# Performance work log

Measured on AMD Instinct MI355X. Metric: run time of the kernel, lower is better.

The kernel has to match this reference:

```python
import jax, jax.numpy as jnp
import numpy as np

DIM = 1024
H = 16          # num query heads
KV = 8          # num kv heads
HD = DIM // H   # head_dim = 64
B, P = 8, 1024


def setup_inputs() -> dict:
    key = jax.random.key(0)
    ks = jax.random.split(key, 6)
    s = 0.02
    return {
        "x": jax.random.normal(ks[0], (B, P, DIM), dtype=jnp.float32),
        "Wq": jax.random.normal(ks[1], (DIM, DIM), dtype=jnp.float32) * s,
        "Wk": jax.random.normal(ks[2], (KV * HD, DIM), dtype=jnp.float32) * s,
        "Wv": jax.random.normal(ks[3], (KV * HD, DIM), dtype=jnp.float32) * s,
        "Wp": jax.random.normal(ks[4], (DIM, DIM), dtype=jnp.float32) * s,
        "bp": jax.random.normal(ks[5], (DIM,), dtype=jnp.float32) * s,
    }


def _q_allocations(k):
    # k: (B, KV, P, HD). k_norms: frobenius norm over (P, HD), summed over batch.
    kn = jnp.sqrt(jnp.sum(k * k, axis=(2, 3))).sum(axis=0)  # (KV,)
    kn = (kn - kn.min()) / (kn.max() - kn.min())
    alloc = jnp.round(kn / kn.sum() * H).astype(jnp.int32)   # (KV,)
    # fix up so alloc.sum() == H (mirrors the torch while-loops)
    alloc = jax.lax.while_loop(lambda a: a.sum() > H,
                               lambda a: a.at[jnp.argmax(a)].add(-1), alloc)
    alloc = jax.lax.while_loop(lambda a: a.sum() < H,
                               lambda a: a.at[jnp.argmin(a)].add(1), alloc)
    return alloc


def reference(x, Wq, Wk, Wv, Wp, bp):
    Bx, Px, C = x.shape
    scale = HD ** -0.5
    q = (x @ Wq.T).reshape(Bx, Px, H, HD).transpose(0, 2, 1, 3) * scale  # (B,H,P,HD)
    k = (x @ Wk.T).reshape(Bx, Px, KV, HD).transpose(0, 2, 1, 3)         # (B,KV,P,HD)
    v = (x @ Wv.T).reshape(Bx, Px, KV, HD).transpose(0, 2, 1, 3)

    alloc = _q_allocations(k)  # (KV,) sums to H
    # query head h belongs to kv group i where cumsum[i-1] <= h < cumsum[i].
    # Equivalent to torch.split(q, alloc) + per-group attention, because the
    # per-group softmax over keys is independent per query head.
    kv_idx = jnp.searchsorted(jnp.cumsum(alloc), jnp.arange(H), side='right')
    k_g = jnp.take(k, kv_idx, axis=1)  # (B,H,P,HD)
    v_g = jnp.take(v, kv_idx, axis=1)

    scores = jnp.einsum('bhqd,bhkd->bhqk', q, k_g)
    weights = jax.nn.softmax(scores, axis=-1)
    out = jnp.einsum('bhqk,bhkd->bhqd', weights, v_g)  # (B,H,P,HD)
    out = out.transpose(0, 2, 1, 3).reshape(Bx, Px, C)
    return out @ Wp.T + bp
```

## Files before the change

### kernel.cpp

```cpp
#include <hip/hip_runtime.h>
#include <stdint.h>


typedef float f32x4 __attribute__((ext_vector_type(4)));
typedef short s16x8 __attribute__((ext_vector_type(8)));
typedef short s16x4 __attribute__((ext_vector_type(4)));
typedef int   i32x4 __attribute__((ext_vector_type(4)));

__device__ __forceinline__ unsigned short f2bf(float f) {
  unsigned int u = __builtin_bit_cast(unsigned int, f);
  u = (u + 0x7FFFu + ((u >> 16) & 1u)) >> 16;
  return (unsigned short)u;
}

__device__ __forceinline__ unsigned int pk_bf16(float a, float b) {
#if __has_builtin(__builtin_amdgcn_cvt_pk_bf16_f32)
  auto v = __builtin_amdgcn_cvt_pk_bf16_f32(a, b);
  return __builtin_bit_cast(unsigned int, v);
#else
  unsigned int ua = __builtin_bit_cast(unsigned int, a);
  unsigned int ub = __builtin_bit_cast(unsigned int, b);
  ua += 0x7FFFu + ((ua >> 16) & 1u);
  ub += 0x7FFFu + ((ub >> 16) & 1u);
#if __has_builtin(__builtin_amdgcn_perm)
  return __builtin_amdgcn_perm(ub, ua, 0x07060302);
#else
  return (ua >> 16) | (ub & 0xFFFF0000u);
#endif
#endif
}

__device__ __forceinline__ unsigned int perm_half(unsigned int hi, unsigned int lo, int takeHi) {
#if __has_builtin(__builtin_amdgcn_perm)
  return __builtin_amdgcn_perm(hi, lo, takeHi ? 0x07060302u : 0x05040100u);
#else
  return takeHi ? ((lo >> 16) | (hi & 0xFFFF0000u)) : ((lo & 0xFFFFu) | (hi << 16));
#endif
}

__device__ __forceinline__ float fast_exp2(float x) {
#if __has_builtin(__builtin_amdgcn_exp2f)
  return __builtin_amdgcn_exp2f(x);
#else
  return exp2f(x);
#endif
}

#if __has_builtin(__builtin_amdgcn_global_load_lds)
#define HAVE_GLL 1
typedef const __attribute__((address_space(1))) void* gas_ptr;
typedef __attribute__((address_space(3))) void* las_ptr;
__device__ __forceinline__ void gll16(const void* g, void* l) {
  __builtin_amdgcn_global_load_lds((gas_ptr)g, (las_ptr)l, 16, 0, 0);
}
#endif

__global__ void convert_kernel(const float* __restrict__ x, const float* __restrict__ Wq,
                               const float* __restrict__ Wk, const float* __restrict__ Wv,
                               const float* __restrict__ Wp,
                               unsigned short* __restrict__ xb,
                               unsigned short* __restrict__ wqkv,
                               unsigned short* __restrict__ wpb,
                               float* __restrict__ sums) {
  if (blockIdx.x == 0 && threadIdx.x < 64) sums[threadIdx.x] = 0.0f;
  const long i = ((long)blockIdx.x * 256 + threadIdx.x) * 4;
  const float* src; unsigned short* dst; long off; float scale = 1.0f;
  if (i < 8388608L)       { src = x;  dst = xb;             off = i;             }
  else if (i < 9437184L)  { src = Wq; dst = wqkv;           off = i - 8388608L;  scale = 0.18033688011112042f; }
  else if (i < 9961472L)  { src = Wk; dst = wqkv + 1048576; off = i - 9437184L;  }
  else if (i < 10485760L) { src = Wv; dst = wqkv + 1572864; off = i - 9961472L;  }
  else                    { src = Wp; dst = wpb;            off = i - 10485760L; }
  f32x4 v = *(const f32x4*)(src + off);
  s16x4 o;
  o[0] = (short)f2bf(v[0] * scale);
  o[1] = (short)f2bf(v[1] * scale);
  o[2] = (short)f2bf(v[2] * scale);
  o[3] = (short)f2bf(v[3] * scale);
  *(s16x4*)(dst + off) = o;
}

template<int N, bool OUT_BF16, bool DO_SUMSQ>
__global__ __launch_bounds__(256)
void gemm_bt(const unsigned short* __restrict__ A,
             const unsigned short* __restrict__ Bw,
             unsigned short* __restrict__ Cb,
             float* __restrict__ Cf,
             const float* __restrict__ bias,
             float* __restrict__ sums) {
  __shared__ __align__(16) unsigned short As[8192];
  __shared__ __align__(16) unsigned short Bs[8192];
  constexpr int NB = N / 128;
  const int bm = blockIdx.x / NB, bn = blockIdx.x % NB;
  const int m0 = bm * 128, n0 = bn * 128;
  const int t = threadIdx.x;
  const int w = t >> 6, lane = t & 63, quad = lane >> 4, ln = lane & 15;
  const int wm = w & 1, wn = w >> 1;

  const int lrow = lane >> 3;
  const int lc8  = ((lane & 7) ^ lrow) << 3;
  const unsigned short* agl = A  + (m0 + w * 32 + lrow) * 1024 + lc8;
  const unsigned short* bgl = Bw + (n0 + w * 32 + lrow) * 1024 + lc8;

  f32x4 acc[4][4] = {};

  for (int k0 = 0; k0 < 1024; k0 += 64) {
    __syncthreads();
#ifdef HAVE_GLL
    #pragma unroll
    for (int c = 0; c < 4; ++c) {
      gll16(agl + k0 + c * 8192, &As[w * 2048 + c * 512]);
      gll16(bgl + k0 + c * 8192, &Bs[w * 2048 + c * 512]);
    }
#else
    i32x4 ra[4], rb[4];
    #pragma unroll
    for (int c = 0; c < 4; ++c) {
      ra[c] = *(const i32x4*)(agl + k0 + c * 8192);
      rb[c] = *(const i32x4*)(bgl + k0 + c * 8192);
    }
    #pragma unroll
    for (int c = 0; c < 4; ++c) {
      *(i32x4*)(&As[w * 2048 + c * 512 + lane * 8]) = ra[c];
      *(i32x4*)(&Bs[w * 2048 + c * 512 + lane * 8]) = rb[c];
    }
#endif
    __syncthreads();
    #pragma unroll
    for (int kc = 0; kc < 2; ++kc) {
      const int pcs = ((kc * 4 + quad) ^ (ln & 7)) << 3;
      s16x8 af[4], bf[4];
      #pragma unroll
      for (int i = 0; i < 4; ++i)
        af[i] = *(const s16x8*)(&As[(wm * 64 + i * 16 + ln) * 64 + pcs]);
      #pragma unroll
      for (int j = 0; j < 4; ++j)
        bf[j] = *(const s16x8*)(&Bs[(wn * 64 + j * 16 + ln) * 64 + pcs]);
      #pragma unroll
      for (int i = 0; i < 4; ++i)
        #pragma unroll
        for (int j = 0; j < 4; ++j)
          acc[i][j] = __builtin_amdgcn_mfma_f32_16x16x32_bf16(af[i], bf[j], acc[i][j], 0, 0, 0);
    }
  }

  if constexpr (DO_SUMSQ) {
    if (bn >= 8 && bn < 12) {
      float ss = 0.0f;
      #pragma unroll
      for (int i = 0; i < 4; ++i)
        #pragma unroll
        for (int j = 0; j < 4; ++j)
          #pragma unroll
          for (int r = 0; r < 4; ++r)
            ss += acc[i][j][r] * acc[i][j][r];
      #pragma unroll
      for (int off = 1; off < 64; off <<= 1) ss += __shfl_xor(ss, off);
      if (lane == 0)
        atomicAdd(&sums[(m0 >> 10) * 8 + (bn - 8) * 2 + wn], ss);
    }
  }

  #pragma unroll
  for (int j = 0; j < 4; ++j) {
    const int gn = n0 + wn * 64 + j * 16 + ln;
    float bv = 0.0f;
    if constexpr (!OUT_BF16) bv = bias[gn];
    #pragma unroll
    for (int i = 0; i < 4; ++i) {
      const int gm0 = m0 + wm * 64 + i * 16 + quad * 4;
      #pragma unroll
      for (int r = 0; r < 4; ++r) {
        float v = acc[i][j][r];
        if constexpr (OUT_BF16) Cb[(gm0 + r) * N + gn] = f2bf(v);
        else                    Cf[(gm0 + r) * N + gn] = v + bv;
      }
    }
  }
}

__global__ __launch_bounds__(256, 4)
void attn_kernel(const unsigned short* __restrict__ qkv,
                 const float* __restrict__ sums,
                 unsigned short* __restrict__ att) {
  __shared__ __align__(16) unsigned short Ks[4096];
  __shared__ __align__(16) unsigned short Vt[64][72];
  __shared__ __align__(16) unsigned int  Plb[4][32][36];
  __shared__ int kvs;

  const int bid = blockIdx.x;
  const int h = bid & 15, qt = (bid >> 4) & 7, b = bid >> 7;
  const int t = threadIdx.x, w = t >> 6, lane = t & 63, quad = lane >> 4, ln = lane & 15;

  if (t == 0) {
    float kn[8];
    for (int kv = 0; kv < 8; ++kv) {
      float s = 0.0f;
      for (int bb = 0; bb < 8; ++bb) s += sqrtf(sums[bb * 8 + kv]);
      kn[kv] = s;
    }
    float mn = kn[0], mx = kn[0];
    for (int i = 1; i < 8; ++i) { mn = fminf(mn, kn[i]); mx = fmaxf(mx, kn[i]); }
    float tot = 0.0f;
    for (int i = 0; i < 8; ++i) { kn[i] = (kn[i] - mn) / (mx - mn); tot += kn[i]; }
    int a[8], sum = 0;
    for (int i = 0; i < 8; ++i) { a[i] = (int)rintf(kn[i] * 16.0f / tot); sum += a[i]; }
    while (sum > 16) {
      int im = 0;
      for (int i = 1; i < 8; ++i) if (a[i] > a[im]) im = i;
      a[im]--; sum--;
    }
    while (sum < 16) {
      int im = 0;
      for (int i = 1; i < 8; ++i) if (a[i] < a[im]) im = i;
      a[im]++; sum++;
    }
    int cum = 0, idx = 0, c[8];
    for (int i = 0; i < 8; ++i) { cum += a[i]; c[i] = cum; }
    while (c[idx] <= h) idx++;
    kvs = idx;
  }
  __syncthreads();
  const int kvi = kvs;

  s16x8 qf[2][2];
  #pragma unroll
  for (int s = 0; s < 2; ++s) {
    const unsigned short* qp = qkv + (b * 1024 + qt * 128 + s * 64 + w * 16 + ln) * 2048
                               + h * 64 + quad * 8;
    qf[s][0] = *(const s16x8*)(qp);
    qf[s][1] = *(const s16x8*)(qp + 32);
  }

  const int lc8 = ((lane & 7) ^ (lane >> 3)) << 3;
  const unsigned short* kglA = qkv + (b * 1024 + w * 16 + (lane >> 3)) * 2048
                               + 1024 + kvi * 64 + lc8;
  const unsigned short* kglB = kglA + 8 * 2048;

  const int kp = t & 31, vd0 = (t >> 5) << 3;
  const unsigned short* vbase = qkv + (b * 1024 + 2 * kp) * 2048 + 1536 + kvi * 64 + vd0;

  s16x8 ones;
  #pragma unroll
  for (int j = 0; j < 8; ++j) ones[j] = (short)0x3F80;

  f32x4 Oa[2][4] = {};
  f32x4 lacc[2] = {};

  s16x8 va0 = *(const s16x8*)(vbase);
  s16x8 va1 = *(const s16x8*)(vbase + 2048);

  for (int kt = 0; kt < 16; ++kt) {
    __syncthreads();
#ifdef HAVE_GLL
    gll16(kglA + kt * 131072, Ks + w * 1024);
    gll16(kglB + kt * 131072, Ks + w * 1024 + 512);
#else
    i32x4 t0 = *(const i32x4*)(kglA + kt * 131072);
    i32x4 t1 = *(const i32x4*)(kglB + kt * 131072);
    *(i32x4*)(Ks + w * 1024 + lane * 8) = t0;
    *(i32x4*)(Ks + w * 1024 + 512 + lane * 8) = t1;
#endif
    #pragma unroll
    for (int i = 0; i < 8; ++i) {
      unsigned int pk = (unsigned int)(unsigned short)va0[i] |
                        ((unsigned int)(unsigned short)va1[i] << 16);
      *(unsigned int*)(&Vt[vd0 + i][2 * kp]) = pk;
    }
    __syncthreads();

    if (kt < 15) {
      const unsigned short* q = vbase + (kt + 1) * 131072;
      va0 = *(const s16x8*)(q);
      va1 = *(const s16x8*)(q + 2048);
    }

    s16x8 kfr[2][4];
    #pragma unroll
    for (int ks = 0; ks < 4; ++ks) {
      const int r0 = (ks * 16 + ln) * 64;
      kfr[0][ks] = *(const s16x8*)(Ks + r0 + (((quad    ) ^ (ln & 7)) << 3));
      kfr[1][ks] = *(const s16x8*)(Ks + r0 + (((quad + 4) ^ (ln & 7)) << 3));
    }

    #pragma unroll
    for (int s = 0; s < 2; ++s) {
      f32x4 sacc[4] = {};
      #pragma unroll
      for (int ks = 0; ks < 4; ++ks) {
        sacc[ks] = __builtin_amdgcn_mfma_f32_16x16x32_bf16(qf[s][0], kfr[0][ks], sacc[ks], 0, 0, 0);
        sacc[ks] = __builtin_amdgcn_mfma_f32_16x16x32_bf16(qf[s][1], kfr[1][ks], sacc[ks], 0, 0, 0);
      }
      #pragma unroll
      for (int r = 0; r < 4; ++r) {
        unsigned int d0 = pk_bf16(fast_exp2(sacc[0][r]), fast_exp2(sacc[1][r]));
        unsigned int d1 = pk_bf16(fast_exp2(sacc[2][r]), fast_exp2(sacc[3][r]));
        unsigned int* pr = &Plb[w][s * 16 + quad * 4 + r][0];
        pr[ln]      = d0;
        pr[ln + 16] = d1;
      }
    }
    __asm__ volatile("s_waitcnt lgkmcnt(0)" ::: "memory");

    #pragma unroll
    for (int kc = 0; kc < 2; ++kc) {
      s16x8 pf[2];
      #pragma unroll
      for (int s = 0; s < 2; ++s) {
        const unsigned int* base = &Plb[w][s * 16 + ln][kc * 16 + (quad & 1) * 8];
        i32x4 u0 = *(const i32x4*)(base);
        i32x4 u1 = *(const i32x4*)(base + 4);
        const int th = quad >> 1;
        i32x4 pp;
        pp[0] = (int)perm_half((unsigned)u0[1], (unsigned)u0[0], th);
        pp[1] = (int)perm_half((unsigned)u0[3], (unsigned)u0[2], th);
        pp[2] = (int)perm_half((unsigned)u1[1], (unsigned)u1[0], th);
        pp[3] = (int)perm_half((unsigned)u1[3], (unsigned)u1[2], th);
        pf[s] = __builtin_bit_cast(s16x8, pp);
      }
      #pragma unroll
      for (int ds = 0; ds < 4; ++ds) {
        s16x8 vf = *(const s16x8*)(&Vt[ds * 16 + ln][kc * 32 + quad * 8]);
        Oa[0][ds] = __builtin_amdgcn_mfma_f32_16x16x32_bf16(pf[0], vf, Oa[0][ds], 0, 0, 0);
        Oa[1][ds] = __builtin_amdgcn_mfma_f32_16x16x32_bf16(pf[1], vf, Oa[1][ds], 0, 0, 0);
      }
      lacc[0] = __builtin_amdgcn_mfma_f32_16x16x32_bf16(pf[0], ones, lacc[0], 0, 0, 0);
      lacc[1] = __builtin_amdgcn_mfma_f32_16x16x32_bf16(pf[1], ones, lacc[1], 0, 0, 0);
    }
  }

  #pragma unroll
  for (int s = 0; s < 2; ++s) {
    float inv[4];
    #pragma unroll
    for (int r = 0; r < 4; ++r) inv[r] = 1.0f / lacc[s][r];
    const int orow = b * 1024 + qt * 128 + s * 64 + w * 16 + quad * 4;
    #pragma unroll
    for (int ds = 0; ds < 4; ++ds)
      #pragma unroll
      for (int r = 0; r < 4; ++r)
        att[(orow + r) * 1024 + h * 64 + ds * 16 + ln] = f2bf(Oa[s][ds][r] * inv[r]);
  }
}

extern "C" void kernel_launch(void* const* d_in, const int* in_sizes, int n_in,
                              void* d_out, int out_size, void* d_ws, size_t ws_size,
                              hipStream_t stream) {
  const float* x  = (const float*)d_in[0];
  const float* Wq = (const float*)d_in[1];
  const float* Wk = (const float*)d_in[2];
  const float* Wv = (const float*)d_in[3];
  const float* Wp = (const float*)d_in[4];
  const float* bp = (const float*)d_in[5];

  char* ws = (char*)d_ws;
  unsigned short* xb   = (unsigned short*)(ws);
  unsigned short* wqkv = (unsigned short*)(ws + 16777216);
  unsigned short* wpb  = (unsigned short*)(ws + 20971520);
  unsigned short* qkv  = (unsigned short*)(ws + 23068672);
  float*          sums = (float*)(ws + 56623104);
  unsigned short* att  = xb;

  convert_kernel<<<11264, 256, 0, stream>>>(x, Wq, Wk, Wv, Wp, xb, wqkv, wpb, sums);
  gemm_bt<2048, true, true><<<1024, 256, 0, stream>>>(xb, wqkv, qkv, nullptr, nullptr, sums);
  attn_kernel<<<1024, 256, 0, stream>>>(qkv, sums, att);
  gemm_bt<1024, false, false><<<512, 256, 0, stream>>>(att, wpb, nullptr, (float*)d_out, bp, nullptr);
}
```

Baseline: 221.3 us.

## Double-buffer K and V tiles in attention kernel shared memory

Splits the K and transposed-V shared-memory tiles into two buffers so the next key tile's global loads and the V transpose writes are issued before computing on the current tile. The loop needs one barrier per iteration instead of two, and global-to-LDS traffic can overlap with the MFMA work. In exchange LDS use rises and the launch-bounds occupancy hint drops from 4 to 3 blocks per CU, which may lower latency hiding across waves.

```diff
diff --git a/kernel.cpp b/kernel.cpp
--- a/kernel.cpp
+++ b/kernel.cpp
@@ -178,12 +178,12 @@
   }
 }
 
-__global__ __launch_bounds__(256, 4)
+__global__ __launch_bounds__(256, 3)
 void attn_kernel(const unsigned short* __restrict__ qkv,
                  const float* __restrict__ sums,
                  unsigned short* __restrict__ att) {
-  __shared__ __align__(16) unsigned short Ks[4096];
-  __shared__ __align__(16) unsigned short Vt[64][72];
+  __shared__ __align__(16) unsigned short Ks[2][4096];
+  __shared__ __align__(16) unsigned short Vt[2][64][72];
   __shared__ __align__(16) unsigned int  Plb[4][32][36];
   __shared__ int kvs;
 
@@ -248,38 +248,59 @@
 
   s16x8 va0 = *(const s16x8*)(vbase);
   s16x8 va1 = *(const s16x8*)(vbase + 2048);
+#ifdef HAVE_GLL
+  gll16(kglA, &Ks[0][w * 1024]);
+  gll16(kglB, &Ks[0][w * 1024 + 512]);
+#else
+  {
+    i32x4 t0 = *(const i32x4*)(kglA);
+    i32x4 t1 = *(const i32x4*)(kglB);
+    *(i32x4*)(&Ks[0][w * 1024 + lane * 8]) = t0;
+    *(i32x4*)(&Ks[0][w * 1024 + 512 + lane * 8]) = t1;
+  }
+#endif
+  #pragma unroll
+  for (int i = 0; i < 8; ++i) {
+    unsigned int pk = (unsigned int)(unsigned short)va0[i] |
+                      ((unsigned int)(unsigned short)va1[i] << 16);
+    *(unsigned int*)(&Vt[0][vd0 + i][2 * kp]) = pk;
+  }
+  va0 = *(const s16x8*)(vbase + 131072);
+  va1 = *(const s16x8*)(vbase + 131072 + 2048);
+  __syncthreads();
 
   for (int kt = 0; kt < 16; ++kt) {
-    __syncthreads();
+    const int p = kt & 1, np = p ^ 1;
+
+    if (kt < 15) {
 #ifdef HAVE_GLL
-    gll16(kglA + kt * 131072, Ks + w * 1024);
-    gll16(kglB + kt * 131072, Ks + w * 1024 + 512);
-#else
-    i32x4 t0 = *(const i32x4*)(kglA + kt * 131072);
-    i32x4 t1 = *(const i32x4*)(kglB + kt * 131072);
-    *(i32x4*)(Ks + w * 1024 + lane * 8) = t0;
-    *(i32x4*)(Ks + w * 1024 + 512 + lane * 8) = t1;
-#endif
-    #pragma unroll
-    for (int i = 0; i < 8; ++i) {
-      unsigned int pk = (unsigned int)(unsigned short)va0[i] |
-                        ((unsigned int)(unsigned short)va1[i] << 16);
-      *(unsigned int*)(&Vt[vd0 + i][2 * kp]) = pk;
-    }
-    __syncthreads();
-
-    if (kt < 15) {
-      const unsigned short* q = vbase + (kt + 1) * 131072;
-      va0 = *(const s16x8*)(q);
-      va1 = *(const s16x8*)(q + 2048);
+      gll16(kglA + (kt + 1) * 131072, &Ks[np][w * 1024]);
+      gll16(kglB + (kt + 1) * 131072, &Ks[np][w * 1024 + 512]);
+#else
+      i32x4 t0 = *(const i32x4*)(kglA + (kt + 1) * 131072);
+      i32x4 t1 = *(const i32x4*)(kglB + (kt + 1) * 131072);
+      *(i32x4*)(&Ks[np][w * 1024 + lane * 8]) = t0;
+      *(i32x4*)(&Ks[np][w * 1024 + 512 + lane * 8]) = t1;
+#endif
+      #pragma unroll
+      for (int i = 0; i < 8; ++i) {
+        unsigned int pk = (unsigned int)(unsigned short)va0[i] |
+                          ((unsigned int)(unsigned short)va1[i] << 16);
+        *(unsigned int*)(&Vt[np][vd0 + i][2 * kp]) = pk;
+      }
+      if (kt < 14) {
+        const unsigned short* q = vbase + (kt + 2) * 131072;
+        va0 = *(const s16x8*)(q);
+        va1 = *(const s16x8*)(q + 2048);
+      }
     }
 
     s16x8 kfr[2][4];
     #pragma unroll
     for (int ks = 0; ks < 4; ++ks) {
       const int r0 = (ks * 16 + ln) * 64;
-      kfr[0][ks] = *(const s16x8*)(Ks + r0 + (((quad    ) ^ (ln & 7)) << 3));
-      kfr[1][ks] = *(const s16x8*)(Ks + r0 + (((quad + 4) ^ (ln & 7)) << 3));
+      kfr[0][ks] = *(const s16x8*)(&Ks[p][r0 + (((quad    ) ^ (ln & 7)) << 3)]);
+      kfr[1][ks] = *(const s16x8*)(&Ks[p][r0 + (((quad + 4) ^ (ln & 7)) << 3)]);
     }
 
     #pragma unroll
@@ -319,13 +340,15 @@
       }
       #pragma unroll
       for (int ds = 0; ds < 4; ++ds) {
-        s16x8 vf = *(const s16x8*)(&Vt[ds * 16 + ln][kc * 32 + quad * 8]);
+        s16x8 vf = *(const s16x8*)(&Vt[p][ds * 16 + ln][kc * 32 + quad * 8]);
         Oa[0][ds] = __builtin_amdgcn_mfma_f32_16x16x32_bf16(pf[0], vf, Oa[0][ds], 0, 0, 0);
         Oa[1][ds] = __builtin_amdgcn_mfma_f32_16x16x32_bf16(pf[1], vf, Oa[1][ds], 0, 0, 0);
       }
       lacc[0] = __builtin_amdgcn_mfma_f32_16x16x32_bf16(pf[0], ones, lacc[0], 0, 0, 0);
       lacc[1] = __builtin_amdgcn_mfma_f32_16x16x32_bf16(pf[1], ones, lacc[1], 0, 0, 0);
     }
+
+    __syncthreads();
   }
 
   #pragma unroll
```

New measurement: 226.3 us. 1.02x slower.

## Compute transposed attention scores so P feeds PV MFMA straight from registers

Applied to the files above, without the earlier changes.

Swaps the MFMA operand order so S^T and O^T come out in registers in a layout that can feed the PV product directly. The per-wave LDS round trip for the probability matrix (Plb buffer, waitcnt, perm shuffles) goes away. To make this work, K rows are permuted when loaded into LDS. The output store becomes packed 8-byte bf16 writes per lane. This removes LDS traffic and the extra sync inside each key tile, but the correctness of the row permutation mapping is a risk.

```diff
diff --git a/kernel.cpp b/kernel.cpp
--- a/kernel.cpp
+++ b/kernel.cpp
@@ -3,6 +3,7 @@
 
 
 typedef float f32x4 __attribute__((ext_vector_type(4)));
+typedef int   i32x2 __attribute__((ext_vector_type(2)));
 typedef short s16x8 __attribute__((ext_vector_type(8)));
 typedef short s16x4 __attribute__((ext_vector_type(4)));
 typedef int   i32x4 __attribute__((ext_vector_type(4)));
@@ -27,14 +28,6 @@
 #else
   return (ua >> 16) | (ub & 0xFFFF0000u);
 #endif
-#endif
-}
-
-__device__ __forceinline__ unsigned int perm_half(unsigned int hi, unsigned int lo, int takeHi) {
-#if __has_builtin(__builtin_amdgcn_perm)
-  return __builtin_amdgcn_perm(hi, lo, takeHi ? 0x07060302u : 0x05040100u);
-#else
-  return takeHi ? ((lo >> 16) | (hi & 0xFFFF0000u)) : ((lo & 0xFFFFu) | (hi << 16));
 #endif
 }
 
@@ -184,7 +177,6 @@
                  unsigned short* __restrict__ att) {
   __shared__ __align__(16) unsigned short Ks[4096];
   __shared__ __align__(16) unsigned short Vt[64][72];
-  __shared__ __align__(16) unsigned int  Plb[4][32][36];
   __shared__ int kvs;
 
   const int bid = blockIdx.x;
@@ -232,9 +224,12 @@
   }
 
   const int lc8 = ((lane & 7) ^ (lane >> 3)) << 3;
-  const unsigned short* kglA = qkv + (b * 1024 + w * 16 + (lane >> 3)) * 2048
-                               + 1024 + kvi * 64 + lc8;
-  const unsigned short* kglB = kglA + 8 * 2048;
+  const int mA = w * 16 + (lane >> 3);
+  const int mB = mA + 8;
+  const int gA = (mA & 0x20) | ((mA & 0x0C) << 1) | ((mA & 0x10) >> 2) | (mA & 3);
+  const int gB = (mB & 0x20) | ((mB & 0x0C) << 1) | ((mB & 0x10) >> 2) | (mB & 3);
+  const unsigned short* kglA = qkv + (b * 1024 + gA) * 2048 + 1024 + kvi * 64 + lc8;
+  const unsigned short* kglB = qkv + (b * 1024 + gB) * 2048 + 1024 + kvi * 64 + lc8;
 
   const int kp = t & 31, vd0 = (t >> 5) << 3;
   const unsigned short* vbase = qkv + (b * 1024 + 2 * kp) * 2048 + 1536 + kvi * 64 + vd0;
@@ -282,63 +277,51 @@
       kfr[1][ks] = *(const s16x8*)(Ks + r0 + (((quad + 4) ^ (ln & 7)) << 3));
     }
 
+    s16x8 pfs[2][2];
     #pragma unroll
     for (int s = 0; s < 2; ++s) {
       f32x4 sacc[4] = {};
       #pragma unroll
       for (int ks = 0; ks < 4; ++ks) {
-        sacc[ks] = __builtin_amdgcn_mfma_f32_16x16x32_bf16(qf[s][0], kfr[0][ks], sacc[ks], 0, 0, 0);
-        sacc[ks] = __builtin_amdgcn_mfma_f32_16x16x32_bf16(qf[s][1], kfr[1][ks], sacc[ks], 0, 0, 0);
+        sacc[ks] = __builtin_amdgcn_mfma_f32_16x16x32_bf16(kfr[0][ks], qf[s][0], sacc[ks], 0, 0, 0);
+        sacc[ks] = __builtin_amdgcn_mfma_f32_16x16x32_bf16(kfr[1][ks], qf[s][1], sacc[ks], 0, 0, 0);
       }
       #pragma unroll
-      for (int r = 0; r < 4; ++r) {
-        unsigned int d0 = pk_bf16(fast_exp2(sacc[0][r]), fast_exp2(sacc[1][r]));
-        unsigned int d1 = pk_bf16(fast_exp2(sacc[2][r]), fast_exp2(sacc[3][r]));
-        unsigned int* pr = &Plb[w][s * 16 + quad * 4 + r][0];
-        pr[ln]      = d0;
-        pr[ln + 16] = d1;
+      for (int kc = 0; kc < 2; ++kc) {
+        i32x4 pd;
+        pd[0] = (int)pk_bf16(fast_exp2(sacc[2*kc][0]),   fast_exp2(sacc[2*kc][1]));
+        pd[1] = (int)pk_bf16(fast_exp2(sacc[2*kc][2]),   fast_exp2(sacc[2*kc][3]));
+        pd[2] = (int)pk_bf16(fast_exp2(sacc[2*kc+1][0]), fast_exp2(sacc[2*kc+1][1]));
+        pd[3] = (int)pk_bf16(fast_exp2(sacc[2*kc+1][2]), fast_exp2(sacc[2*kc+1][3]));
+        pfs[s][kc] = __builtin_bit_cast(s16x8, pd);
       }
     }
-    __asm__ volatile("s_waitcnt lgkmcnt(0)" ::: "memory");
 
     #pragma unroll
     for (int kc = 0; kc < 2; ++kc) {
-      s16x8 pf[2];
-      #pragma unroll
-      for (int s = 0; s < 2; ++s) {
-        const unsigned int* base = &Plb[w][s * 16 + ln][kc * 16 + (quad & 1) * 8];
-        i32x4 u0 = *(const i32x4*)(base);
-        i32x4 u1 = *(const i32x4*)(base + 4);
-        const int th = quad >> 1;
-        i32x4 pp;
-        pp[0] = (int)perm_half((unsigned)u0[1], (unsigned)u0[0], th);
-        pp[1] = (int)perm_half((unsigned)u0[3], (unsigned)u0[2], th);
-        pp[2] = (int)perm_half((unsigned)u1[1], (unsigned)u1[0], th);
-        pp[3] = (int)perm_half((unsigned)u1[3], (unsigned)u1[2], th);
-        pf[s] = __builtin_bit_cast(s16x8, pp);
-      }
       #pragma unroll
       for (int ds = 0; ds < 4; ++ds) {
         s16x8 vf = *(const s16x8*)(&Vt[ds * 16 + ln][kc * 32 + quad * 8]);
-        Oa[0][ds] = __builtin_amdgcn_mfma_f32_16x16x32_bf16(pf[0], vf, Oa[0][ds], 0, 0, 0);
-        Oa[1][ds] = __builtin_amdgcn_mfma_f32_16x16x32_bf16(pf[1], vf, Oa[1][ds], 0, 0, 0);
+        Oa[0][ds] = __builtin_amdgcn_mfma_f32_16x16x32_bf16(vf, pfs[0][kc], Oa[0][ds], 0, 0, 0);
+        Oa[1][ds] = __builtin_amdgcn_mfma_f32_16x16x32_bf16(vf, pfs[1][kc], Oa[1][ds], 0, 0, 0);
       }
-      lacc[0] = __builtin_amdgcn_mfma_f32_16x16x32_bf16(pf[0], ones, lacc[0], 0, 0, 0);
-      lacc[1] = __builtin_amdgcn_mfma_f32_16x16x32_bf16(pf[1], ones, lacc[1], 0, 0, 0);
+      lacc[0] = __builtin_amdgcn_mfma_f32_16x16x32_bf16(ones, pfs[0][kc], lacc[0], 0, 0, 0);
+      lacc[1] = __builtin_amdgcn_mfma_f32_16x16x32_bf16(ones, pfs[1][kc], lacc[1], 0, 0, 0);
     }
   }
 
   #pragma unroll
   for (int s = 0; s < 2; ++s) {
-    float inv[4];
-    #pragma unroll
-    for (int r = 0; r < 4; ++r) inv[r] = 1.0f / lacc[s][r];
-    const int orow = b * 1024 + qt * 128 + s * 64 + w * 16 + quad * 4;
-    #pragma unroll
-    for (int ds = 0; ds < 4; ++ds)
-      #pragma unroll
-      for (int r = 0; r < 4; ++r)
-        att[(orow + r) * 1024 + h * 64 + ds * 16 + ln] = f2bf(Oa[s][ds][r] * inv[r]);
+    const float inv = 1.0f / lacc[s][0];
+    unsigned short* orow = att + (b * 1024 + qt * 128 + s * 64 + w * 16 + ln) * 1024
+                           + h * 64 + quad * 4;
+    #pragma unroll
+    for (int ds = 0; ds < 4; ++ds) {
+      i32x2 pk;
+      pk[0] = (int)pk_bf16(Oa[s][ds][0] * inv, Oa[s][ds][1] * inv);
+      pk[1] = (int)pk_bf16(Oa[s][ds][2] * inv, Oa[s][ds][3] * inv);
+      *(i32x2*)(orow + ds * 16) = pk;
+    }
   }
 }
 
```

New measurement: 219.2 us. About the same (-0.9%).
